# Optimization experiments

Hardware: AMD Instinct MI355X
Metric: run time of the kernel (lower is better)

The kernel has to match this reference:

```python
import jax, jax.numpy as jnp
import numpy as np

B, C, H, W = 4, 512, 64, 64
CQ = C // 4  # query/key channels


def setup_inputs() -> dict:
    key = jax.random.key(0)
    ks = jax.random.split(key, 8)
    s_in = 1.0 / np.sqrt(C)
    return {
        "x": jax.random.normal(ks[0], (B, C, H, W), dtype=jnp.float32),
        "Wf_w": jax.random.normal(ks[1], (CQ, C), dtype=jnp.float32) * s_in,
        "Wf_b": jax.random.normal(ks[2], (CQ,), dtype=jnp.float32) * 0.01,
        "Wh_w": jax.random.normal(ks[3], (CQ, C), dtype=jnp.float32) * s_in,
        "Wh_b": jax.random.normal(ks[4], (CQ,), dtype=jnp.float32) * 0.01,
        "Wl_w": jax.random.normal(ks[5], (C, C), dtype=jnp.float32) * s_in,
        "Wl_b": jax.random.normal(ks[6], (C,), dtype=jnp.float32) * 0.01,
        "alpha": jax.random.uniform(ks[7], (1,), dtype=jnp.float32),
    }


def reference(x, Wf_w, Wf_b, Wh_w, Wh_b, Wl_w, Wl_b, alpha):
    b, c, h, w = x.shape
    n = h * w
    xr = x.reshape(b, c, n)  # (B, C, N)
    # 1x1 convs == per-pixel linear projections
    f = jnp.einsum('oc,bcn->bon', Wf_w, xr) + Wf_b[None, :, None]  # (B, C/4, N)
    k = jnp.einsum('oc,bcn->bon', Wh_w, xr) + Wh_b[None, :, None]  # (B, C/4, N)
    v = jnp.einsum('oc,bcn->bon', Wl_w, xr) + Wl_b[None, :, None]  # (B, C,   N)
    # t[b, i, j] = <f[:, i], k[:, j]>  -> (B, N, N)
    scores = jnp.einsum('boi,boj->bij', f, k)
    att = jax.nn.softmax(scores, axis=-1)
    # out[b, c, i] = sum_j v[b, c, j] * att[b, i, j]  (bmm with att^T)
    out = jnp.einsum('bcj,bij->bci', v, att)
    out = out.reshape(b, c, h, w)
    return out * alpha[0] + x
```

## Files before the change

kernel.cpp:

```cpp
#include <hip/hip_runtime.h>
#include <hip/hip_bf16.h>

typedef _Float16 f16;
typedef _Float16 f16x4 __attribute__((ext_vector_type(4)));
typedef _Float16 f16x8 __attribute__((ext_vector_type(8)));
typedef float f32x4 __attribute__((ext_vector_type(4)));

constexpr int BATCH = 4, C = 512, CQ = 128, N = 4096;
constexpr int FKD = 256;

constexpr size_t WS_XT   = 0;
constexpr size_t WS_FT   = WS_XT   + (size_t)BATCH * N * C * 2;
constexpr size_t WS_KT   = WS_FT   + (size_t)BATCH * N * CQ * 2;
constexpr size_t WS_V    = WS_KT   + (size_t)BATCH * N * CQ * 2;
constexpr size_t WS_WCAT = WS_V    + (size_t)BATCH * C * N * 2;
constexpr size_t WS_WL   = WS_WCAT + (size_t)FKD * C * 2;
constexpr size_t WS_BC   = WS_WL   + (size_t)C * C * 2;

__global__ void prep_weights(const float* __restrict__ Wf_w, const float* __restrict__ Wf_b,
                             const float* __restrict__ Wh_w, const float* __restrict__ Wh_b,
                             const float* __restrict__ Wl_w,
                             f16* __restrict__ wcat, f16* __restrict__ wl, float* __restrict__ bcat) {
    int i = blockIdx.x * 256 + threadIdx.x;
    if (i < FKD * C) {
        int o = i >> 9, c = i & 511;
        float v = (o < CQ) ? Wf_w[o * C + c] : Wh_w[(o - CQ) * C + c];
        wcat[i] = (f16)v;
    }
    if (i < C * C) wl[i] = (f16)Wl_w[i];
    if (i < FKD) bcat[i] = (i < CQ) ? Wf_b[i] : Wh_b[i - CQ];
}

__global__ void transpose_x(const float* __restrict__ x, f16* __restrict__ xt) {
    __shared__ float tile[64][65];
    int gid = blockIdx.x;
    int b = gid >> 9, rem = gid & 511;
    int c0 = (rem >> 6) * 64, n0 = (rem & 63) * 64;
    int t = threadIdx.x;
    int tn = t & 63, tg = t >> 6;
    const float* xp = x + (size_t)b * C * N + (size_t)c0 * N + n0;
#pragma unroll
    for (int r = 0; r < 16; ++r) {
        int cl = tg + r * 4;
        tile[cl][tn] = xp[(size_t)cl * N + tn];
    }
    __syncthreads();
    f16* xo = xt + (size_t)b * N * C + (size_t)n0 * C + c0;
#pragma unroll
    for (int r = 0; r < 16; ++r) {
        int nl = tg + r * 4;
        xo[(size_t)nl * C + tn] = (f16)tile[tn][nl];
    }
}

__global__ void __launch_bounds__(256) proj_fk(const f16* __restrict__ xt, const f16* __restrict__ wcat,
                                               const float* __restrict__ bcat,
                                               f16* __restrict__ ft, f16* __restrict__ kt) {
    int wid = blockIdx.x * 4 + (threadIdx.x >> 6);
    int lane = threadIdx.x & 63;
    int li = lane & 15, lg = lane >> 4;
    int b  = wid >> 8;
    int nt = (wid >> 2) & 63;
    int ot = wid & 3;
    int n0 = nt * 64, o0 = ot * 64;
    const f16* ap = xt + (size_t)(b * N + n0 + li) * C + lg * 8;
    const f16* bp = wcat + (size_t)(o0 + li) * C + lg * 8;
    f32x4 acc[4][4] = {};
    for (int ks = 0; ks < 16; ++ks) {
        f16x8 a4[4], b4[4];
#pragma unroll
        for (int t = 0; t < 4; ++t) a4[t] = *(const f16x8*)(ap + (size_t)(t * 16) * C + ks * 32);
#pragma unroll
        for (int t = 0; t < 4; ++t) b4[t] = *(const f16x8*)(bp + (size_t)(t * 16) * C + ks * 32);
#pragma unroll
        for (int tA = 0; tA < 4; ++tA)
#pragma unroll
            for (int tB = 0; tB < 4; ++tB)
                acc[tA][tB] = __builtin_amdgcn_mfma_f32_16x16x32_f16(a4[tA], b4[tB], acc[tA][tB], 0, 0, 0);
    }
#pragma unroll
    for (int tB = 0; tB < 4; ++tB) {
        int o = o0 + tB * 16 + li;
        float bias = bcat[o];
        if (o < CQ) {
#pragma unroll
            for (int tA = 0; tA < 4; ++tA)
#pragma unroll
                for (int r = 0; r < 4; ++r) {
                    int n = n0 + tA * 16 + lg * 4 + r;
                    ft[((size_t)(b * N + n)) * CQ + o] = (f16)(acc[tA][tB][r] + bias);
                }
        } else {
            int ck = o - CQ;
#pragma unroll
            for (int tA = 0; tA < 4; ++tA)
#pragma unroll
                for (int r = 0; r < 4; ++r) {
                    int n = n0 + tA * 16 + lg * 4 + r;
                    kt[(((size_t)b * (N >> 2) + (n >> 2)) * 4 + (n & 3)) * 128 + ck] = (f16)(acc[tA][tB][r] + bias);
                }
        }
    }
}

__global__ void __launch_bounds__(256) proj_v(const f16* __restrict__ xt, const f16* __restrict__ wl,
                                              const float* __restrict__ wlb, f16* __restrict__ v) {
    int wid = blockIdx.x * 4 + (threadIdx.x >> 6);
    int lane = threadIdx.x & 63;
    int li = lane & 15, lg = lane >> 4;
    int b  = wid >> 9;
    int ct = (wid >> 6) & 7;
    int nt = wid & 63;
    int c0 = ct * 64, n0 = nt * 64;
    const f16* ap = wl + (size_t)(c0 + li) * C + lg * 8;
    const f16* bp = xt + (size_t)(b * N + n0 + li) * C + lg * 8;
    f32x4 acc[4][4] = {};
    for (int ks = 0; ks < 16; ++ks) {
        f16x8 a4[4], b4[4];
#pragma unroll
        for (int t = 0; t < 4; ++t) a4[t] = *(const f16x8*)(ap + (size_t)(t * 16) * C + ks * 32);
#pragma unroll
        for (int t = 0; t < 4; ++t) b4[t] = *(const f16x8*)(bp + (size_t)(t * 16) * C + ks * 32);
#pragma unroll
        for (int tA = 0; tA < 4; ++tA)
#pragma unroll
            for (int tB = 0; tB < 4; ++tB)
                acc[tA][tB] = __builtin_amdgcn_mfma_f32_16x16x32_f16(a4[tA], b4[tB], acc[tA][tB], 0, 0, 0);
    }
#pragma unroll
    for (int tA = 0; tA < 4; ++tA)
#pragma unroll
        for (int r = 0; r < 4; ++r) {
            int c = c0 + tA * 16 + lg * 4 + r;
            float bias = wlb[c];
            const size_t cpb = ((size_t)b * 32 + (c >> 4)) * 512;
            const int cl = c & 15;
#pragma unroll
            for (int tB = 0; tB < 4; ++tB) {
                int n = n0 + tB * 16 + li;
                v[(cpb + (n >> 3)) * 128 + cl * 8 + (n & 7)] = (f16)(acc[tA][tB][r] + bias);
            }
        }
}

__global__ void __launch_bounds__(512, 2) attn(const f16* __restrict__ ft, const f16* __restrict__ kt,
                                               const f16* __restrict__ v,
                                               const float* __restrict__ x, const float* __restrict__ alphap,
                                               float* __restrict__ out) {
    __shared__ __align__(16) f16 kbuf[2][128 * 128];
    __shared__ __align__(16) f16 pbuf[64 * 128];
    __shared__ float smax[8][4][16];
    __shared__ float ssum[8][4][16];

    const int tid  = threadIdx.x;
    const int wv   = tid >> 6;
    const int lane = tid & 63;
    const int li = lane & 15, lg = lane >> 4;
    const int swl = li & 7;
    const int v0 = blockIdx.x;
    const int b  = (v0 & 7) >> 1;
    const int it = ((v0 & 1) << 5) | (v0 >> 3);
    const int i0 = it * 64;
    const int c0 = wv * 64;

    f16x8 fb[4][4];
#pragma unroll
    for (int f = 0; f < 4; ++f) {
        const f16* fp = ft + (size_t)(b * N + i0 + f * 16 + li) * CQ + lg * 8;
#pragma unroll
        for (int ks = 0; ks < 4; ++ks) fb[f][ks] = *(const f16x8*)(fp + ks * 32);
    }

    const f16* ktb = kt + (size_t)b * N * 128;
    {
#pragma unroll
        for (int k = 0; k < 4; ++k) {
            f16x8 vv = *(const f16x8*)(ktb + (((size_t)(wv * 4 + k)) * 4 + lg) * 128 + li * 8);
            *(f16x8*)(&kbuf[0][(wv * 16 + k * 4 + lg) * 128 + ((li ^ ((k * 4 + lg) & 7)) * 8)]) = vv;
        }
    }

    const f16* vb2 = v + (((size_t)b * 32 + wv * 4) * 512 + lg) * 128 + li * 8;
    f32x4 oacc[4][4] = {};
    float ms[4] = {-1e30f, -1e30f, -1e30f, -1e30f};
    float ls[4] = {0.f, 0.f, 0.f, 0.f};
    __syncthreads();

    for (int t = 0; t < 32; ++t) {
        const f16* kc = &kbuf[t & 1][0];
        f16*       kn = &kbuf[(t + 1) & 1][0];
        const size_t jb0 = (size_t)t * 16;
        const int gn = (t < 31) ? (t + 1) * 32 : 0;
        f16x8 stg[4];
#pragma unroll
        for (int k = 0; k < 4; ++k)
            stg[k] = *(const f16x8*)(ktb + (((size_t)(gn + wv * 4 + k)) * 4 + lg) * 128 + li * 8);

        f16x8 kf4[4];
#pragma unroll
        for (int ks = 0; ks < 4; ++ks)
            kf4[ks] = *(const f16x8*)(&kc[(wv * 16 + li) * 128 + ((ks * 4 + lg) ^ swl) * 8]);
        f32x4 s[4] = {};
        __builtin_amdgcn_s_setprio(1);
#pragma unroll
        for (int ks = 0; ks < 4; ++ks)
#pragma unroll
            for (int f = 0; f < 4; ++f)
                s[f] = __builtin_amdgcn_mfma_f32_16x16x32_f16(kf4[ks], fb[f][ks], s[f], 0, 0, 0);
        __builtin_amdgcn_s_setprio(0);

        float tm[4];
#pragma unroll
        for (int f = 0; f < 4; ++f) {
            float t0 = fmaxf(fmaxf(s[f][0], s[f][1]), fmaxf(s[f][2], s[f][3]));
            t0 = fmaxf(t0, __shfl_xor(t0, 16));
            t0 = fmaxf(t0, __shfl_xor(t0, 32));
            tm[f] = t0;
        }
        if (lane < 16) {
#pragma unroll
            for (int f = 0; f < 4; ++f) smax[wv][f][li] = tm[f];
        }
        f16x8 va[2][4];
#pragma unroll
        for (int cf = 0; cf < 4; ++cf) va[0][cf] = *(const f16x8*)(vb2 + ((size_t)cf * 512 + jb0) * 128);
        __syncthreads();
        float gm[4];
#pragma unroll
        for (int f = 0; f < 4; ++f) {
            float m0 = smax[0][f][li];
#pragma unroll
            for (int w = 1; w < 8; ++w) m0 = fmaxf(m0, smax[w][f][li]);
            gm[f] = m0;
        }
#pragma unroll
        for (int cf = 0; cf < 4; ++cf) va[1][cf] = *(const f16x8*)(vb2 + ((size_t)cf * 512 + jb0 + 4) * 128);
#pragma unroll
        for (int f = 0; f < 4; ++f) {
            if (!__all(gm[f] <= ms[f] + 8.0f)) {
                float mn = fmaxf(ms[f], gm[f]), sc = __expf(ms[f] - mn);
                ms[f] = mn; ls[f] *= sc;
#pragma unroll
                for (int cf = 0; cf < 4; ++cf) oacc[cf][f] *= sc;
            }
        }
        const int jl = wv * 16 + lg * 4;
        const int gg = (jl >> 3) ^ swl;
        float ps[4];
#pragma unroll
        for (int f = 0; f < 4; ++f) {
            f16x4 pk;
            float p0 = 0.f;
#pragma unroll
            for (int r = 0; r < 4; ++r) { float p = __expf(s[f][r] - ms[f]); p0 += p; pk[r] = (f16)p; }
            *(f16x4*)(&pbuf[(f * 16 + li) * 128 + gg * 8 + (jl & 7)]) = pk;
            ps[f] = p0;
        }
#pragma unroll
        for (int f = 0; f < 4; ++f) {
            ps[f] += __shfl_xor(ps[f], 16);
            ps[f] += __shfl_xor(ps[f], 32);
        }
        if (lane < 16) {
#pragma unroll
            for (int f = 0; f < 4; ++f) ssum[wv][f][li] = ps[f];
        }
#pragma unroll
        for (int k = 0; k < 4; ++k)
            *(f16x8*)(&kn[(wv * 16 + k * 4 + lg) * 128 + ((li ^ ((k * 4 + lg) & 7)) * 8)]) = stg[k];
        __syncthreads();
#pragma unroll
        for (int f = 0; f < 4; ++f) {
            float a0 = 0.f;
#pragma unroll
            for (int w = 0; w < 8; ++w) a0 += ssum[w][f][li];
            ls[f] += a0;
        }
#pragma unroll
        for (int kf = 0; kf < 4; ++kf) {
            const int cur = kf & 1;
            const int g = (kf * 4 + lg) ^ swl;
            f16x8 pb[4];
#pragma unroll
            for (int f = 0; f < 4; ++f)
                pb[f] = *(const f16x8*)(&pbuf[(f * 16 + li) * 128 + g * 8]);
            f16x8 vv0 = va[cur][0], vv1 = va[cur][1], vv2 = va[cur][2], vv3 = va[cur][3];
            if (kf < 2) {
#pragma unroll
                for (int cf = 0; cf < 4; ++cf)
                    va[cur][cf] = *(const f16x8*)(vb2 + ((size_t)cf * 512 + jb0 + (kf + 2) * 4) * 128);
            }
            __builtin_amdgcn_s_setprio(1);
#pragma unroll
            for (int f = 0; f < 4; ++f) {
                oacc[0][f] = __builtin_amdgcn_mfma_f32_16x16x32_f16(vv0, pb[f], oacc[0][f], 0, 0, 0);
                oacc[1][f] = __builtin_amdgcn_mfma_f32_16x16x32_f16(vv1, pb[f], oacc[1][f], 0, 0, 0);
                oacc[2][f] = __builtin_amdgcn_mfma_f32_16x16x32_f16(vv2, pb[f], oacc[2][f], 0, 0, 0);
                oacc[3][f] = __builtin_amdgcn_mfma_f32_16x16x32_f16(vv3, pb[f], oacc[3][f], 0, 0, 0);
            }
            __builtin_amdgcn_s_setprio(0);
        }
    }

    const float alpha = alphap[0];
#pragma unroll
    for (int f = 0; f < 4; ++f) {
        const float invf = alpha / ls[f];
        const float* xp = x + (size_t)(b * C + c0) * N + i0 + f * 16 + li;
        float* op = out + (size_t)(b * C + c0) * N + i0 + f * 16 + li;
#pragma unroll
        for (int cf = 0; cf < 4; ++cf)
#pragma unroll
            for (int r = 0; r < 4; ++r) {
                const int cl = cf * 16 + lg * 4 + r;
                op[(size_t)cl * N] = oacc[cf][f][r] * invf + xp[(size_t)cl * N];
            }
    }
}

extern "C" void kernel_launch(void* const* d_in, const int* in_sizes, int n_in,
                              void* d_out, int out_size, void* d_ws, size_t ws_size,
                              hipStream_t stream) {
    const float* x     = (const float*)d_in[0];
    const float* Wf_w  = (const float*)d_in[1];
    const float* Wf_b  = (const float*)d_in[2];
    const float* Wh_w  = (const float*)d_in[3];
    const float* Wh_b  = (const float*)d_in[4];
    const float* Wl_w  = (const float*)d_in[5];
    const float* Wl_b  = (const float*)d_in[6];
    const float* alpha = (const float*)d_in[7];
    char* ws = (char*)d_ws;
    f16*   xt   = (f16*)(ws + WS_XT);
    f16*   ftb  = (f16*)(ws + WS_FT);
    f16*   ktb  = (f16*)(ws + WS_KT);
    f16*   vb   = (f16*)(ws + WS_V);
    f16*   wcat = (f16*)(ws + WS_WCAT);
    f16*   wl   = (f16*)(ws + WS_WL);
    float* bcat = (float*)(ws + WS_BC);
    float* out  = (float*)d_out;

    prep_weights<<<dim3((C * C + 255) / 256), dim3(256), 0, stream>>>(Wf_w, Wf_b, Wh_w, Wh_b, Wl_w, wcat, wl, bcat);
    transpose_x<<<dim3(BATCH * 8 * 64), dim3(256), 0, stream>>>(x, xt);
    proj_fk<<<dim3(256), dim3(256), 0, stream>>>(xt, wcat, bcat, ftb, ktb);
    proj_v<<<dim3(512), dim3(256), 0, stream>>>(xt, wl, Wl_b, vb);
    attn<<<dim3(256), dim3(512), 0, stream>>>(ftb, ktb, vb, x, alpha, out);
}
```

Measured before the change: 188.3 us.

## Switch attention kernel to 32x32x16 MFMA with 4x2 wave tiling

The attention kernel moves from 16x16x32 MFMA tiles to 32x32x16 MFMA tiles. The 8 waves are reorganised as 4 column groups by 2 query-row groups. Each wave now owns 32 query rows and 128 output channels and handles one row max and one row sum instead of four. The aim is fewer MFMA issues, fewer per-row reductions and shuffles, and a smaller shared-memory reduction footprint. In exchange, V and P access patterns change and K fragments are now read from LDS inside the MFMA loop, which may cost more latency or bank conflicts.

```diff
diff --git a/kernel.cpp b/kernel.cpp
--- a/kernel.cpp
+++ b/kernel.cpp
@@ -5,6 +5,7 @@
 typedef _Float16 f16x4 __attribute__((ext_vector_type(4)));
 typedef _Float16 f16x8 __attribute__((ext_vector_type(8)));
 typedef float f32x4 __attribute__((ext_vector_type(4)));
+typedef float f32x16 __attribute__((ext_vector_type(16)));
 
 constexpr int BATCH = 4, C = 512, CQ = 128, N = 4096;
 constexpr int FKD = 256;
@@ -149,26 +150,27 @@
                                                float* __restrict__ out) {
     __shared__ __align__(16) f16 kbuf[2][128 * 128];
     __shared__ __align__(16) f16 pbuf[64 * 128];
-    __shared__ float smax[8][4][16];
-    __shared__ float ssum[8][4][16];
+    __shared__ float smax[4][2][32];
+    __shared__ float ssum[4][2][32];
 
     const int tid  = threadIdx.x;
     const int wv   = tid >> 6;
     const int lane = tid & 63;
     const int li = lane & 15, lg = lane >> 4;
-    const int swl = li & 7;
+    const int l31 = lane & 31, lh = lane >> 5;
+    const int sw = l31 & 7;
+    const int wj = wv & 3;
+    const int wi = wv >> 2;
     const int v0 = blockIdx.x;
     const int b  = (v0 & 7) >> 1;
     const int it = ((v0 & 1) << 5) | (v0 >> 3);
     const int i0 = it * 64;
-    const int c0 = wv * 64;
-
-    f16x8 fb[4][4];
-#pragma unroll
-    for (int f = 0; f < 4; ++f) {
-        const f16* fp = ft + (size_t)(b * N + i0 + f * 16 + li) * CQ + lg * 8;
-#pragma unroll
-        for (int ks = 0; ks < 4; ++ks) fb[f][ks] = *(const f16x8*)(fp + ks * 32);
+
+    f16x8 fb[8];
+    {
+        const f16* fp = ft + (size_t)(b * N + i0 + wi * 32 + l31) * CQ + lh * 8;
+#pragma unroll
+        for (int ks = 0; ks < 8; ++ks) fb[ks] = *(const f16x8*)(fp + ks * 16);
     }
 
     const f16* ktb = kt + (size_t)b * N * 128;
@@ -180,142 +182,98 @@
         }
     }
 
-    const f16* vb2 = v + (((size_t)b * 32 + wv * 4) * 512 + lg) * 128 + li * 8;
-    f32x4 oacc[4][4] = {};
-    float ms[4] = {-1e30f, -1e30f, -1e30f, -1e30f};
-    float ls[4] = {0.f, 0.f, 0.f, 0.f};
+    const f16* vL = v + (((size_t)b * 32 + wj * 8 + (l31 >> 4)) * 512 + lh) * 128 + (l31 & 15) * 8;
+    const int prow = wi * 32 + l31;
+    f32x16 oacc[4] = {};
+    float ms = -1e30f, ls = 0.f;
     __syncthreads();
 
     for (int t = 0; t < 32; ++t) {
         const f16* kc = &kbuf[t & 1][0];
         f16*       kn = &kbuf[(t + 1) & 1][0];
-        const size_t jb0 = (size_t)t * 16;
         const int gn = (t < 31) ? (t + 1) * 32 : 0;
         f16x8 stg[4];
 #pragma unroll
         for (int k = 0; k < 4; ++k)
             stg[k] = *(const f16x8*)(ktb + (((size_t)(gn + wv * 4 + k)) * 4 + lg) * 128 + li * 8);
 
-        f16x8 kf4[4];
-#pragma unroll
-        for (int ks = 0; ks < 4; ++ks)
-            kf4[ks] = *(const f16x8*)(&kc[(wv * 16 + li) * 128 + ((ks * 4 + lg) ^ swl) * 8]);
-        f32x4 s[4] = {};
+        f32x16 s = {};
         __builtin_amdgcn_s_setprio(1);
 #pragma unroll
-        for (int ks = 0; ks < 4; ++ks)
-#pragma unroll
-            for (int f = 0; f < 4; ++f)
-                s[f] = __builtin_amdgcn_mfma_f32_16x16x32_f16(kf4[ks], fb[f][ks], s[f], 0, 0, 0);
+        for (int ks = 0; ks < 8; ++ks) {
+            f16x8 kf = *(const f16x8*)(&kc[(wj * 32 + l31) * 128 + (((ks * 2 + lh) ^ sw) * 8)]);
+            s = __builtin_amdgcn_mfma_f32_32x32x16_f16(kf, fb[ks], s, 0, 0, 0);
+        }
         __builtin_amdgcn_s_setprio(0);
 
-        float tm[4];
-#pragma unroll
-        for (int f = 0; f < 4; ++f) {
-            float t0 = fmaxf(fmaxf(s[f][0], s[f][1]), fmaxf(s[f][2], s[f][3]));
-            t0 = fmaxf(t0, __shfl_xor(t0, 16));
-            t0 = fmaxf(t0, __shfl_xor(t0, 32));
-            tm[f] = t0;
-        }
-        if (lane < 16) {
-#pragma unroll
-            for (int f = 0; f < 4; ++f) smax[wv][f][li] = tm[f];
-        }
-        f16x8 va[2][4];
-#pragma unroll
-        for (int cf = 0; cf < 4; ++cf) va[0][cf] = *(const f16x8*)(vb2 + ((size_t)cf * 512 + jb0) * 128);
+        float tm = s[0];
+#pragma unroll
+        for (int r = 1; r < 16; ++r) tm = fmaxf(tm, s[r]);
+        tm = fmaxf(tm, __shfl_xor(tm, 32));
+        if (lane < 32) smax[wj][wi][l31] = tm;
+        f16x8 vaA[4], vaB[4];
+#pragma unroll
+        for (int ct = 0; ct < 4; ++ct) vaA[ct] = *(const f16x8*)(vL + ((size_t)(ct * 1024 + t * 16)) * 128);
         __syncthreads();
-        float gm[4];
-#pragma unroll
-        for (int f = 0; f < 4; ++f) {
-            float m0 = smax[0][f][li];
-#pragma unroll
-            for (int w = 1; w < 8; ++w) m0 = fmaxf(m0, smax[w][f][li]);
-            gm[f] = m0;
-        }
-#pragma unroll
-        for (int cf = 0; cf < 4; ++cf) va[1][cf] = *(const f16x8*)(vb2 + ((size_t)cf * 512 + jb0 + 4) * 128);
-#pragma unroll
-        for (int f = 0; f < 4; ++f) {
-            if (!__all(gm[f] <= ms[f] + 8.0f)) {
-                float mn = fmaxf(ms[f], gm[f]), sc = __expf(ms[f] - mn);
-                ms[f] = mn; ls[f] *= sc;
-#pragma unroll
-                for (int cf = 0; cf < 4; ++cf) oacc[cf][f] *= sc;
-            }
-        }
-        const int jl = wv * 16 + lg * 4;
-        const int gg = (jl >> 3) ^ swl;
-        float ps[4];
-#pragma unroll
-        for (int f = 0; f < 4; ++f) {
+        float gm = fmaxf(fmaxf(smax[0][wi][l31], smax[1][wi][l31]),
+                         fmaxf(smax[2][wi][l31], smax[3][wi][l31]));
+        if (!__all(gm <= ms + 8.0f)) {
+            float mn = fmaxf(ms, gm), sc = __expf(ms - mn);
+            ms = mn; ls *= sc;
+#pragma unroll
+            for (int ct = 0; ct < 4; ++ct) oacc[ct] *= sc;
+        }
+#pragma unroll
+        for (int ct = 0; ct < 4; ++ct) vaB[ct] = *(const f16x8*)(vL + ((size_t)(ct * 1024 + t * 16 + 2)) * 128);
+        float psum = 0.f;
+#pragma unroll
+        for (int q = 0; q < 4; ++q) {
             f16x4 pk;
-            float p0 = 0.f;
-#pragma unroll
-            for (int r = 0; r < 4; ++r) { float p = __expf(s[f][r] - ms[f]); p0 += p; pk[r] = (f16)p; }
-            *(f16x4*)(&pbuf[(f * 16 + li) * 128 + gg * 8 + (jl & 7)]) = pk;
-            ps[f] = p0;
-        }
-#pragma unroll
-        for (int f = 0; f < 4; ++f) {
-            ps[f] += __shfl_xor(ps[f], 16);
-            ps[f] += __shfl_xor(ps[f], 32);
-        }
-        if (lane < 16) {
-#pragma unroll
-            for (int f = 0; f < 4; ++f) ssum[wv][f][li] = ps[f];
-        }
+#pragma unroll
+            for (int r = 0; r < 4; ++r) { float p = __expf(s[q * 4 + r] - ms); psum += p; pk[r] = (f16)p; }
+            const int g = (wj * 4 + q) ^ sw;
+            *(f16x4*)(&pbuf[prow * 128 + g * 8 + lh * 4]) = pk;
+        }
+        psum += __shfl_xor(psum, 32);
+        if (lane < 32) ssum[wj][wi][l31] = psum;
 #pragma unroll
         for (int k = 0; k < 4; ++k)
             *(f16x8*)(&kn[(wv * 16 + k * 4 + lg) * 128 + ((li ^ ((k * 4 + lg) & 7)) * 8)]) = stg[k];
         __syncthreads();
-#pragma unroll
-        for (int f = 0; f < 4; ++f) {
-            float a0 = 0.f;
-#pragma unroll
-            for (int w = 0; w < 8; ++w) a0 += ssum[w][f][li];
-            ls[f] += a0;
-        }
-#pragma unroll
-        for (int kf = 0; kf < 4; ++kf) {
-            const int cur = kf & 1;
-            const int g = (kf * 4 + lg) ^ swl;
-            f16x8 pb[4];
-#pragma unroll
-            for (int f = 0; f < 4; ++f)
-                pb[f] = *(const f16x8*)(&pbuf[(f * 16 + li) * 128 + g * 8]);
-            f16x8 vv0 = va[cur][0], vv1 = va[cur][1], vv2 = va[cur][2], vv3 = va[cur][3];
-            if (kf < 2) {
-#pragma unroll
-                for (int cf = 0; cf < 4; ++cf)
-                    va[cur][cf] = *(const f16x8*)(vb2 + ((size_t)cf * 512 + jb0 + (kf + 2) * 4) * 128);
+        ls += ssum[0][wi][l31] + ssum[1][wi][l31] + ssum[2][wi][l31] + ssum[3][wi][l31];
+#pragma unroll
+        for (int js = 0; js < 8; ++js) {
+            f16x8 pb = *(const f16x8*)(&pbuf[prow * 128 + (((js * 2 + lh) ^ sw) * 8)]);
+            f16x8 vv0, vv1, vv2, vv3;
+            if (js & 1) { vv0 = vaB[0]; vv1 = vaB[1]; vv2 = vaB[2]; vv3 = vaB[3]; }
+            else        { vv0 = vaA[0]; vv1 = vaA[1]; vv2 = vaA[2]; vv3 = vaA[3]; }
+            if (js < 6) {
+#pragma unroll
+                for (int ct = 0; ct < 4; ++ct) {
+                    f16x8 nv = *(const f16x8*)(vL + ((size_t)(ct * 1024 + t * 16 + (js + 2) * 2)) * 128);
+                    if (js & 1) vaB[ct] = nv; else vaA[ct] = nv;
+                }
             }
             __builtin_amdgcn_s_setprio(1);
-#pragma unroll
-            for (int f = 0; f < 4; ++f) {
-                oacc[0][f] = __builtin_amdgcn_mfma_f32_16x16x32_f16(vv0, pb[f], oacc[0][f], 0, 0, 0);
-                oacc[1][f] = __builtin_amdgcn_mfma_f32_16x16x32_f16(vv1, pb[f], oacc[1][f], 0, 0, 0);
-                oacc[2][f] = __builtin_amdgcn_mfma_f32_16x16x32_f16(vv2, pb[f], oacc[2][f], 0, 0, 0);
-                oacc[3][f] = __builtin_amdgcn_mfma_f32_16x16x32_f16(vv3, pb[f], oacc[3][f], 0, 0, 0);
-            }
+            oacc[0] = __builtin_amdgcn_mfma_f32_32x32x16_f16(vv0, pb, oacc[0], 0, 0, 0);
+            oacc[1] = __builtin_amdgcn_mfma_f32_32x32x16_f16(vv1, pb, oacc[1], 0, 0, 0);
+            oacc[2] = __builtin_amdgcn_mfma_f32_32x32x16_f16(vv2, pb, oacc[2], 0, 0, 0);
+            oacc[3] = __builtin_amdgcn_mfma_f32_32x32x16_f16(vv3, pb, oacc[3], 0, 0, 0);
             __builtin_amdgcn_s_setprio(0);
         }
     }
 
     const float alpha = alphap[0];
-#pragma unroll
-    for (int f = 0; f < 4; ++f) {
-        const float invf = alpha / ls[f];
-        const float* xp = x + (size_t)(b * C + c0) * N + i0 + f * 16 + li;
-        float* op = out + (size_t)(b * C + c0) * N + i0 + f * 16 + li;
-#pragma unroll
-        for (int cf = 0; cf < 4; ++cf)
-#pragma unroll
-            for (int r = 0; r < 4; ++r) {
-                const int cl = cf * 16 + lg * 4 + r;
-                op[(size_t)cl * N] = oacc[cf][f][r] * invf + xp[(size_t)cl * N];
-            }
-    }
+    const float inv = alpha / ls;
+    const int icol = i0 + wi * 32 + l31;
+#pragma unroll
+    for (int ct = 0; ct < 4; ++ct)
+#pragma unroll
+        for (int r = 0; r < 16; ++r) {
+            const int c = wj * 128 + ct * 32 + (r & 3) + 8 * (r >> 2) + 4 * lh;
+            const size_t off = (size_t)(b * C + c) * N + icol;
+            out[off] = oacc[ct][r] * inv + x[off];
+        }
 }
 
 extern "C" void kernel_launch(void* const* d_in, const int* in_sizes, int n_in,
```

After: 190.3 us. Within noise of the previous version (+1.1%).

## Fuse x transpose and all three projections into one kernel

Applied to the files above, without the earlier changes.

Removes the separate transpose_x kernel and the fp16 xt workspace. A single proj_all kernel now stages each 64-channel chunk of x through shared memory, converting to fp16 and transposing on the fly. It also computes the f, k and v projections together from one concatenated 768-row weight matrix. This cuts launches and avoids writing and rereading the transposed x, but each block reads its weights directly from global memory with no LDS reuse, and the LDS stores during staging are strided per thread.

```diff
diff --git a/kernel.cpp b/kernel.cpp
--- a/kernel.cpp
+++ b/kernel.cpp
@@ -7,140 +7,90 @@
 typedef float f32x4 __attribute__((ext_vector_type(4)));
 
 constexpr int BATCH = 4, C = 512, CQ = 128, N = 4096;
-constexpr int FKD = 256;
-
-constexpr size_t WS_XT   = 0;
-constexpr size_t WS_FT   = WS_XT   + (size_t)BATCH * N * C * 2;
+constexpr int OALL = 768;
+
+constexpr size_t WS_FT   = 0;
 constexpr size_t WS_KT   = WS_FT   + (size_t)BATCH * N * CQ * 2;
 constexpr size_t WS_V    = WS_KT   + (size_t)BATCH * N * CQ * 2;
-constexpr size_t WS_WCAT = WS_V    + (size_t)BATCH * C * N * 2;
-constexpr size_t WS_WL   = WS_WCAT + (size_t)FKD * C * 2;
-constexpr size_t WS_BC   = WS_WL   + (size_t)C * C * 2;
+constexpr size_t WS_WALL = WS_V    + (size_t)BATCH * C * N * 2;
+constexpr size_t WS_BALL = WS_WALL + (size_t)OALL * C * 2;
 
 __global__ void prep_weights(const float* __restrict__ Wf_w, const float* __restrict__ Wf_b,
                              const float* __restrict__ Wh_w, const float* __restrict__ Wh_b,
-                             const float* __restrict__ Wl_w,
-                             f16* __restrict__ wcat, f16* __restrict__ wl, float* __restrict__ bcat) {
+                             const float* __restrict__ Wl_w, const float* __restrict__ Wl_b,
+                             f16* __restrict__ wall, float* __restrict__ ball) {
     int i = blockIdx.x * 256 + threadIdx.x;
-    if (i < FKD * C) {
+    if (i < OALL * C) {
         int o = i >> 9, c = i & 511;
-        float v = (o < CQ) ? Wf_w[o * C + c] : Wh_w[(o - CQ) * C + c];
-        wcat[i] = (f16)v;
-    }
-    if (i < C * C) wl[i] = (f16)Wl_w[i];
-    if (i < FKD) bcat[i] = (i < CQ) ? Wf_b[i] : Wh_b[i - CQ];
-}
-
-__global__ void transpose_x(const float* __restrict__ x, f16* __restrict__ xt) {
-    __shared__ float tile[64][65];
-    int gid = blockIdx.x;
-    int b = gid >> 9, rem = gid & 511;
-    int c0 = (rem >> 6) * 64, n0 = (rem & 63) * 64;
-    int t = threadIdx.x;
-    int tn = t & 63, tg = t >> 6;
-    const float* xp = x + (size_t)b * C * N + (size_t)c0 * N + n0;
-#pragma unroll
-    for (int r = 0; r < 16; ++r) {
-        int cl = tg + r * 4;
-        tile[cl][tn] = xp[(size_t)cl * N + tn];
-    }
-    __syncthreads();
-    f16* xo = xt + (size_t)b * N * C + (size_t)n0 * C + c0;
-#pragma unroll
-    for (int r = 0; r < 16; ++r) {
-        int nl = tg + r * 4;
-        xo[(size_t)nl * C + tn] = (f16)tile[tn][nl];
-    }
-}
-
-__global__ void __launch_bounds__(256) proj_fk(const f16* __restrict__ xt, const f16* __restrict__ wcat,
-                                               const float* __restrict__ bcat,
-                                               f16* __restrict__ ft, f16* __restrict__ kt) {
-    int wid = blockIdx.x * 4 + (threadIdx.x >> 6);
-    int lane = threadIdx.x & 63;
-    int li = lane & 15, lg = lane >> 4;
-    int b  = wid >> 8;
-    int nt = (wid >> 2) & 63;
-    int ot = wid & 3;
-    int n0 = nt * 64, o0 = ot * 64;
-    const f16* ap = xt + (size_t)(b * N + n0 + li) * C + lg * 8;
-    const f16* bp = wcat + (size_t)(o0 + li) * C + lg * 8;
-    f32x4 acc[4][4] = {};
-    for (int ks = 0; ks < 16; ++ks) {
-        f16x8 a4[4], b4[4];
-#pragma unroll
-        for (int t = 0; t < 4; ++t) a4[t] = *(const f16x8*)(ap + (size_t)(t * 16) * C + ks * 32);
-#pragma unroll
-        for (int t = 0; t < 4; ++t) b4[t] = *(const f16x8*)(bp + (size_t)(t * 16) * C + ks * 32);
-#pragma unroll
-        for (int tA = 0; tA < 4; ++tA)
-#pragma unroll
-            for (int tB = 0; tB < 4; ++tB)
-                acc[tA][tB] = __builtin_amdgcn_mfma_f32_16x16x32_f16(a4[tA], b4[tB], acc[tA][tB], 0, 0, 0);
-    }
-#pragma unroll
-    for (int tB = 0; tB < 4; ++tB) {
-        int o = o0 + tB * 16 + li;
-        float bias = bcat[o];
-        if (o < CQ) {
-#pragma unroll
-            for (int tA = 0; tA < 4; ++tA)
-#pragma unroll
-                for (int r = 0; r < 4; ++r) {
-                    int n = n0 + tA * 16 + lg * 4 + r;
-                    ft[((size_t)(b * N + n)) * CQ + o] = (f16)(acc[tA][tB][r] + bias);
+        float v = (o < 128) ? Wf_w[o * C + c]
+                : (o < 256) ? Wh_w[(o - 128) * C + c]
+                            : Wl_w[(o - 256) * C + c];
+        wall[i] = (f16)v;
+    }
+    if (i < OALL)
+        ball[i] = (i < 128) ? Wf_b[i] : (i < 256) ? Wh_b[i - 128] : Wl_b[i - 256];
+}
+
+__global__ void __launch_bounds__(512) proj_all(const float* __restrict__ x, const f16* __restrict__ wall,
+                                                const float* __restrict__ ball,
+                                                f16* __restrict__ ft, f16* __restrict__ kt,
+                                                f16* __restrict__ v) {
+    __shared__ __align__(16) f16 xl[64][72];
+    const int tid = threadIdx.x;
+    const int wv  = tid >> 6;
+    const int lane = tid & 63;
+    const int li = lane & 15, lg = lane >> 4;
+    const int b  = blockIdx.x >> 6;
+    const int n0 = (blockIdx.x & 63) * 64;
+    const int ob = wv * 96;
+    const int nn = tid & 63, cg = tid >> 6;
+
+    f32x4 acc[6][4] = {};
+    for (int ch = 0; ch < 8; ++ch) {
+        __syncthreads();
+        {
+            const float* xs = x + ((size_t)(b * C) + ch * 64 + cg * 8) * N + n0 + nn;
+#pragma unroll
+            for (int r = 0; r < 8; ++r)
+                xl[nn][cg * 8 + r] = (f16)xs[(size_t)r * N];
+        }
+        __syncthreads();
+#pragma unroll
+        for (int ks = 0; ks < 2; ++ks) {
+            f16x8 xfr[4];
+#pragma unroll
+            for (int nf = 0; nf < 4; ++nf)
+                xfr[nf] = *(const f16x8*)(&xl[nf * 16 + li][ks * 32 + lg * 8]);
+#pragma unroll
+            for (int of = 0; of < 6; ++of) {
+                f16x8 wfr = *(const f16x8*)(wall + (size_t)(ob + of * 16 + li) * C + ch * 64 + ks * 32 + lg * 8);
+#pragma unroll
+                for (int nf = 0; nf < 4; ++nf)
+                    acc[of][nf] = __builtin_amdgcn_mfma_f32_16x16x32_f16(xfr[nf], wfr, acc[of][nf], 0, 0, 0);
+            }
+        }
+    }
+#pragma unroll
+    for (int of = 0; of < 6; ++of) {
+        const int o = ob + of * 16 + li;
+        const float bias = ball[o];
+#pragma unroll
+        for (int nf = 0; nf < 4; ++nf)
+#pragma unroll
+            for (int r = 0; r < 4; ++r) {
+                const int n = n0 + nf * 16 + lg * 4 + r;
+                const f16 val = (f16)(acc[of][nf][r] + bias);
+                if (o < 128) {
+                    ft[(size_t)(b * N + n) * CQ + o] = val;
+                } else if (o < 256) {
+                    const int ck = o - 128;
+                    kt[(((size_t)b * (N >> 2) + (n >> 2)) * 4 + (n & 3)) * 128 + ck] = val;
+                } else {
+                    const int c = o - 256;
+                    v[(((size_t)b * 32 + (c >> 4)) * 512 + (n >> 3)) * 128 + (c & 15) * 8 + (n & 7)] = val;
                 }
-        } else {
-            int ck = o - CQ;
-#pragma unroll
-            for (int tA = 0; tA < 4; ++tA)
-#pragma unroll
-                for (int r = 0; r < 4; ++r) {
-                    int n = n0 + tA * 16 + lg * 4 + r;
-                    kt[(((size_t)b * (N >> 2) + (n >> 2)) * 4 + (n & 3)) * 128 + ck] = (f16)(acc[tA][tB][r] + bias);
-                }
-        }
-    }
-}
-
-__global__ void __launch_bounds__(256) proj_v(const f16* __restrict__ xt, const f16* __restrict__ wl,
-                                              const float* __restrict__ wlb, f16* __restrict__ v) {
-    int wid = blockIdx.x * 4 + (threadIdx.x >> 6);
-    int lane = threadIdx.x & 63;
-    int li = lane & 15, lg = lane >> 4;
-    int b  = wid >> 9;
-    int ct = (wid >> 6) & 7;
-    int nt = wid & 63;
-    int c0 = ct * 64, n0 = nt * 64;
-    const f16* ap = wl + (size_t)(c0 + li) * C + lg * 8;
-    const f16* bp = xt + (size_t)(b * N + n0 + li) * C + lg * 8;
-    f32x4 acc[4][4] = {};
-    for (int ks = 0; ks < 16; ++ks) {
-        f16x8 a4[4], b4[4];
-#pragma unroll
-        for (int t = 0; t < 4; ++t) a4[t] = *(const f16x8*)(ap + (size_t)(t * 16) * C + ks * 32);
-#pragma unroll
-        for (int t = 0; t < 4; ++t) b4[t] = *(const f16x8*)(bp + (size_t)(t * 16) * C + ks * 32);
-#pragma unroll
-        for (int tA = 0; tA < 4; ++tA)
-#pragma unroll
-            for (int tB = 0; tB < 4; ++tB)
-                acc[tA][tB] = __builtin_amdgcn_mfma_f32_16x16x32_f16(a4[tA], b4[tB], acc[tA][tB], 0, 0, 0);
-    }
-#pragma unroll
-    for (int tA = 0; tA < 4; ++tA)
-#pragma unroll
-        for (int r = 0; r < 4; ++r) {
-            int c = c0 + tA * 16 + lg * 4 + r;
-            float bias = wlb[c];
-            const size_t cpb = ((size_t)b * 32 + (c >> 4)) * 512;
-            const int cl = c & 15;
-#pragma unroll
-            for (int tB = 0; tB < 4; ++tB) {
-                int n = n0 + tB * 16 + li;
-                v[(cpb + (n >> 3)) * 128 + cl * 8 + (n & 7)] = (f16)(acc[tA][tB][r] + bias);
-            }
-        }
+            }
+    }
 }
 
 __global__ void __launch_bounds__(512, 2) attn(const f16* __restrict__ ft, const f16* __restrict__ kt,
@@ -330,18 +280,14 @@
     const float* Wl_b  = (const float*)d_in[6];
     const float* alpha = (const float*)d_in[7];
     char* ws = (char*)d_ws;
-    f16*   xt   = (f16*)(ws + WS_XT);
     f16*   ftb  = (f16*)(ws + WS_FT);
     f16*   ktb  = (f16*)(ws + WS_KT);
     f16*   vb   = (f16*)(ws + WS_V);
-    f16*   wcat = (f16*)(ws + WS_WCAT);
-    f16*   wl   = (f16*)(ws + WS_WL);
-    float* bcat = (float*)(ws + WS_BC);
+    f16*   wall = (f16*)(ws + WS_WALL);
+    float* ball = (float*)(ws + WS_BALL);
     float* out  = (float*)d_out;
 
-    prep_weights<<<dim3((C * C + 255) / 256), dim3(256), 0, stream>>>(Wf_w, Wf_b, Wh_w, Wh_b, Wl_w, wcat, wl, bcat);
-    transpose_x<<<dim3(BATCH * 8 * 64), dim3(256), 0, stream>>>(x, xt);
-    proj_fk<<<dim3(256), dim3(256), 0, stream>>>(xt, wcat, bcat, ftb, ktb);
-    proj_v<<<dim3(512), dim3(256), 0, stream>>>(xt, wl, Wl_b, vb);
+    prep_weights<<<dim3((OALL * C + 255) / 256), dim3(256), 0, stream>>>(Wf_w, Wf_b, Wh_w, Wh_b, Wl_w, Wl_b, wall, ball);
+    proj_all<<<dim3(256), dim3(512), 0, stream>>>(x, wall, ball, ftb, ktb, vb);
     attn<<<dim3(256), dim3(512), 0, stream>>>(ftb, ktb, vb, x, alpha, out);
 }
```

Measured after the change: 167.9 us. 1.12x faster.
